# Performance work log

Hardware: AMD Instinct MI355X
Metric: run time of the kernel (lower is better)

Reference implementation:

```python
import jax, jax.numpy as jnp
import numpy as np

RES = 2048
IN = 3
OUT = 2
THRESHOLD = 1.0
BETA = 0.9
SPECTRAL_RADIUS = 0.9


def _make_W(rng):
    # random recurrent matrix scaled to target spectral radius (power iteration estimate)
    W = rng.standard_normal((RES, RES)).astype(np.float32)
    v = rng.standard_normal(RES).astype(np.float32)
    lam = 1.0
    for _ in range(100):
        v = W @ v
        lam = np.linalg.norm(v)
        v = v / (lam + 1e-12)
    return W * (SPECTRAL_RADIUS / lam)


def _xavier(rng, fan_out, fan_in):
    bound = np.sqrt(6.0 / (fan_in + fan_out))
    return rng.uniform(-bound, bound, (fan_out, fan_in)).astype(np.float32)


def setup_inputs() -> dict:
    key = jax.random.key(0)
    rng = np.random.default_rng(42)
    x = jax.random.normal(key, (200, 256, IN), dtype=jnp.float32)
    W = jnp.asarray(_make_W(rng))            # [RES, RES] recurrent weights
    Win = jnp.asarray(_xavier(rng, RES, IN))  # [RES, IN]  input_layer.weight
    Wout = jnp.asarray(_xavier(rng, OUT, RES))  # [OUT, RES] readout.weight
    return {"x": x, "W": W, "Win": Win, "Wout": Wout}


def reference(x, W, Win, Wout):
    seq_len, batch, _ = x.shape
    res = W.shape[0]

    def step(carry, x_t):
        V, S = carry
        # leaky integrate: input current + recurrent current
        V_new = BETA * V + x_t @ Win.T + S @ W  # [batch, res]
        S_new = (V_new >= THRESHOLD).astype(V.dtype)
        V_new = V_new * (1.0 - S_new)  # reset_mechanism == 'zero'
        return (V_new, S_new), S_new

    init = (jnp.zeros((batch, res), x.dtype), jnp.zeros((batch, res), x.dtype))
    _, spk_rec = jax.lax.scan(step, init, x)  # [seq, batch, res]
    spk_avg = spk_rec[-10:].mean(axis=0)       # [batch, res]
    logits = spk_avg @ Wout.T                  # [batch, out]
    return spk_rec, logits
```

## Files before the change

kernel.cpp:

```cpp
#include <hip/hip_runtime.h>


#define SEQ    200
#define BATCH  256
#define NRES   2048
#define NTHR   1024
#define BETA_F 0.9f

__global__ __launch_bounds__(NTHR, 1) void snn_reservoir_kernel(
    const float* __restrict__ x,
    const float* __restrict__ W,
    const float* __restrict__ Win,
    const float* __restrict__ Wout,
    float* __restrict__ out)
{
    const int b    = blockIdx.x;
    const int tid  = threadIdx.x;
    const int lane = tid & 63;
    const int wid  = tid >> 6;
    const int n0   = tid << 1;

    __shared__ unsigned long long smask[2][32];
    __shared__ int    scum[2];
    __shared__ float4 sx[SEQ];
    __shared__ float  red[2][16];
    __shared__ int    sspike;

    for (int t = tid; t < SEQ; t += NTHR) {
        const float* p = x + (size_t)t * (BATCH * 3) + b * 3;
        sx[t] = make_float4(p[0], p[1], p[2], 0.0f);
    }
    if (tid == 0) sspike = 0;

    const float* wr = Win + (size_t)n0 * 3;
    const float w00 = wr[0], w01 = wr[1], w02 = wr[2];
    const float w10 = wr[3], w11 = wr[4], w12 = wr[5];

    __syncthreads();

    float V0 = 0.f, V1 = 0.f;
    bool  any = false;
    unsigned long long* pout =
        (unsigned long long*)(out + (size_t)b * NRES + n0);
    const size_t step_ull = (size_t)BATCH * NRES / 2;

    #pragma unroll 4
    for (int t = 0; t < SEQ; ++t) {
        const float4 xv = sx[t];
        const float i0 = fmaf(xv.x, w00, fmaf(xv.y, w01, xv.z * w02));
        const float i1 = fmaf(xv.x, w10, fmaf(xv.y, w11, xv.z * w12));
        V0 = fmaf(BETA_F, V0, i0);
        V1 = fmaf(BETA_F, V1, i1);
        const bool s0 = (V0 >= 1.0f);
        const bool s1 = (V1 >= 1.0f);
        any |= (s0 | s1);
        V0 = s0 ? 0.f : V0;
        V1 = s1 ? 0.f : V1;
        const unsigned long long wv =
            ((unsigned long long)(s1 ? 0x3f800000u : 0u) << 32) |
            (unsigned long long)(s0 ? 0x3f800000u : 0u);
        __builtin_nontemporal_store(wv, pout);
        pout += step_ull;
    }

    const int wany = __any(any);
    if (wany && lane == 0) atomicOr(&sspike, 1);
    __syncthreads();

    const size_t loff = (size_t)SEQ * BATCH * NRES;
    if (sspike == 0) {
        if (tid == 0) {
            out[loff + b * 2 + 0] = 0.f;
            out[loff + b * 2 + 1] = 0.f;
        }
        return;
    }

    if (tid < 64) smask[tid >> 5][tid & 31] = 0ull;
    if (tid < 2)  scum[tid] = 0;
    V0 = 0.f; V1 = 0.f;
    int cnt0 = 0, cnt1 = 0;
    __syncthreads();

    auto step = [&](int t, int cur, int prev, int& seen) {
        float rec0 = 0.f, rec1 = 0.f;
        const int c = scum[prev];
        if (__builtin_expect(c != seen, 0)) {
            seen = c;
            #pragma unroll 1
            for (int u = 0; u < 32; ++u) {
                unsigned long long m = smask[prev][u];
                const int kbase = ((u >> 1) << 7) + (u & 1);
                while (m) {
                    const int l = __builtin_ctzll(m);
                    m &= m - 1;
                    const int k = kbase + (l << 1);
                    const float2 wvv = *(const float2*)(W + (size_t)k * NRES + n0);
                    rec0 += wvv.x;
                    rec1 += wvv.y;
                }
            }
        }
        const float4 xv = sx[t];
        const float i0 = fmaf(xv.x, w00, fmaf(xv.y, w01, xv.z * w02)) + rec0;
        const float i1 = fmaf(xv.x, w10, fmaf(xv.y, w11, xv.z * w12)) + rec1;
        V0 = fmaf(BETA_F, V0, i0);
        V1 = fmaf(BETA_F, V1, i1);
        const bool s0 = (V0 >= 1.0f);
        const bool s1 = (V1 >= 1.0f);
        V0 = s0 ? 0.f : V0;
        V1 = s1 ? 0.f : V1;
        *(float2*)(out + ((size_t)t * BATCH + b) * NRES + n0) =
            make_float2(s0 ? 1.f : 0.f, s1 ? 1.f : 0.f);
        if (t >= SEQ - 10) { cnt0 += (int)s0; cnt1 += (int)s1; }
        const unsigned long long b0 = __ballot(s0);
        const unsigned long long b1 = __ballot(s1);
        if (lane == 0) {
            smask[cur][2 * wid]     = b0;
            smask[cur][2 * wid + 1] = b1;
            const int pc = __popcll(b0) + __popcll(b1);
            if (pc) atomicAdd(&scum[cur], pc);
        }
        asm volatile("s_waitcnt lgkmcnt(0)\n\ts_barrier" ::: "memory");
    };

    int seen0 = 0, seen1 = 0;
    for (int tt = 0; tt < SEQ; tt += 2) {
        step(tt,     0, 1, seen1);
        step(tt + 1, 1, 0, seen0);
    }

    const float a0 = (float)cnt0 * 0.1f;
    const float a1 = (float)cnt1 * 0.1f;
    float p0 = fmaf(a0, Wout[n0], a1 * Wout[n0 + 1]);
    float p1 = fmaf(a0, Wout[NRES + n0], a1 * Wout[NRES + n0 + 1]);
    #pragma unroll
    for (int off = 32; off > 0; off >>= 1) {
        p0 += __shfl_down(p0, off);
        p1 += __shfl_down(p1, off);
    }
    if (lane == 0) { red[0][wid] = p0; red[1][wid] = p1; }
    __syncthreads();
    if (tid == 0) {
        float q0 = 0.f, q1 = 0.f;
        #pragma unroll
        for (int i = 0; i < 16; ++i) { q0 += red[0][i]; q1 += red[1][i]; }
        out[loff + b * 2 + 0] = q0;
        out[loff + b * 2 + 1] = q1;
    }
}

extern "C" void kernel_launch(void* const* d_in, const int* in_sizes, int n_in,
                              void* d_out, int out_size, void* d_ws, size_t ws_size,
                              hipStream_t stream) {
    const float* x    = (const float*)d_in[0];
    const float* W    = (const float*)d_in[1];
    const float* Win  = (const float*)d_in[2];
    const float* Wout = (const float*)d_in[3];
    float* out = (float*)d_out;
    hipLaunchKernelGGL(snn_reservoir_kernel, dim3(BATCH), dim3(NTHR), 0, stream,
                       x, W, Win, Wout, out);
}
```

Measured before the change: 425.6 us.

## Screen for spike-free inputs with a bound check and stream zeros bandwidth-optimally

Adds a tiny scan kernel that computes the leak-filtered input trace per (t, batch) row, plus a conservative bound using the max |Win| per input channel. A wide grid-stride kernel writes the whole spike and logit output as float4 zeros. Rows whose bound can reach threshold get an exact per-neuron potential check, which raises a global flag. The full recurrent kernel runs only when that flag is set. This replaces the old write path, which used one block per batch element and strided 8-byte nontemporal stores, with a fully coalesced wide write. The cost is extra launches and a small serial scan, and the full kernel still launches every time and returns early when the flag is clear.

```diff
diff --git a/kernel.cpp b/kernel.cpp
--- a/kernel.cpp
+++ b/kernel.cpp
@@ -4,16 +4,113 @@
 #define SEQ    200
 #define BATCH  256
 #define NRES   2048
-#define NTHR   1024
 #define BETA_F 0.9f
-
-__global__ __launch_bounds__(NTHR, 1) void snn_reservoir_kernel(
+#define NROW   (SEQ * BATCH)
+#define SPK_FLOATS ((size_t)SEQ * BATCH * NRES)
+#define LOGITS 512
+#define WS_FLOATS (64 + NROW + 3 * NROW)
+
+__global__ __launch_bounds__(256) void scan_kernel(
+    const float* __restrict__ x,
+    const float* __restrict__ Win,
+    float* __restrict__ ws)
+{
+    __shared__ float swm[4][3];
+    __shared__ float wm[3];
+    const int tid  = threadIdx.x;
+    const int lane = tid & 63;
+    const int wv   = tid >> 6;
+
+    float p0 = 0.f, p1 = 0.f, p2 = 0.f;
+    for (int n = tid; n < NRES; n += 256) {
+        const float* r = Win + (size_t)n * 3;
+        p0 = fmaxf(p0, fabsf(r[0]));
+        p1 = fmaxf(p1, fabsf(r[1]));
+        p2 = fmaxf(p2, fabsf(r[2]));
+    }
+    #pragma unroll
+    for (int off = 32; off; off >>= 1) {
+        p0 = fmaxf(p0, __shfl_down(p0, off));
+        p1 = fmaxf(p1, __shfl_down(p1, off));
+        p2 = fmaxf(p2, __shfl_down(p2, off));
+    }
+    if (lane == 0) { swm[wv][0] = p0; swm[wv][1] = p1; swm[wv][2] = p2; }
+    __syncthreads();
+    if (tid == 0) {
+        wm[0] = fmaxf(fmaxf(swm[0][0], swm[1][0]), fmaxf(swm[2][0], swm[3][0]));
+        wm[1] = fmaxf(fmaxf(swm[0][1], swm[1][1]), fmaxf(swm[2][1], swm[3][1]));
+        wm[2] = fmaxf(fmaxf(swm[0][2], swm[1][2]), fmaxf(swm[2][2], swm[3][2]));
+        if (blockIdx.x == 0) *(int*)ws = 0;
+    }
+    __syncthreads();
+
+    if (tid < 64) {
+        const int b = blockIdx.x * 64 + tid;
+        const float w0 = wm[0], w1 = wm[1], w2 = wm[2];
+        float* rowbound = ws + 64;
+        float* xs       = ws + 64 + NROW;
+        float X0 = 0.f, X1 = 0.f, X2 = 0.f;
+        #pragma unroll 4
+        for (int t = 0; t < SEQ; ++t) {
+            const float* px = x + ((size_t)t * BATCH + b) * 3;
+            X0 = fmaf(BETA_F, X0, px[0]);
+            X1 = fmaf(BETA_F, X1, px[1]);
+            X2 = fmaf(BETA_F, X2, px[2]);
+            const int r = t * BATCH + b;
+            rowbound[r] = fmaf(fabsf(X0), w0, fmaf(fabsf(X1), w1, fabsf(X2) * w2));
+            float* xr = xs + (size_t)r * 3;
+            xr[0] = X0; xr[1] = X1; xr[2] = X2;
+        }
+    }
+}
+
+__global__ __launch_bounds__(256) void stream_kernel(
+    const float* __restrict__ Win,
+    float* __restrict__ out,
+    float* __restrict__ ws)
+{
+    const float* rowbound = ws + 64;
+    const float* xs       = ws + 64 + NROW;
+    int* flag = (int*)ws;
+    const size_t nspk   = SPK_FLOATS / 4;
+    const size_t nchunk = nspk + LOGITS / 4;
+    const size_t stride = (size_t)gridDim.x * blockDim.x;
+    size_t idx = (size_t)blockIdx.x * blockDim.x + threadIdx.x;
+    const float4 z = make_float4(0.f, 0.f, 0.f, 0.f);
+
+    for (; idx < nchunk; idx += stride) {
+        if (idx < nspk) {
+            const int r = (int)(idx >> 9);
+            const float bnd = rowbound[r];
+            if (__builtin_expect(!(bnd < 0.999f), 0)) {
+                const int n = ((int)idx & 511) << 2;
+                const float* X = xs + (size_t)r * 3;
+                const float X0 = X[0], X1 = X[1], X2 = X[2];
+                const float* wr = Win + (size_t)n * 3;
+                const float v0 = fmaf(X0, wr[0], fmaf(X1, wr[1],  X2 * wr[2]));
+                const float v1 = fmaf(X0, wr[3], fmaf(X1, wr[4],  X2 * wr[5]));
+                const float v2 = fmaf(X0, wr[6], fmaf(X1, wr[7],  X2 * wr[8]));
+                const float v3 = fmaf(X0, wr[9], fmaf(X1, wr[10], X2 * wr[11]));
+                if (!(v0 < 1.f) || !(v1 < 1.f) || !(v2 < 1.f) || !(v3 < 1.f))
+                    atomicOr(flag, 1);
+            }
+        }
+        reinterpret_cast<float4*>(out)[idx] = z;
+    }
+}
+
+#define NTHR 1024
+
+__global__ __launch_bounds__(NTHR, 1) void fallback_kernel(
     const float* __restrict__ x,
     const float* __restrict__ W,
     const float* __restrict__ Win,
     const float* __restrict__ Wout,
-    float* __restrict__ out)
+    float* __restrict__ out,
+    const float* __restrict__ ws)
 {
+    if (*(const int*)ws == 0) return;
+
     const int b    = blockIdx.x;
     const int tid  = threadIdx.x;
     const int lane = tid & 63;
@@ -24,61 +121,19 @@
     __shared__ int    scum[2];
     __shared__ float4 sx[SEQ];
     __shared__ float  red[2][16];
-    __shared__ int    sspike;
 
     for (int t = tid; t < SEQ; t += NTHR) {
         const float* p = x + (size_t)t * (BATCH * 3) + b * 3;
         sx[t] = make_float4(p[0], p[1], p[2], 0.0f);
     }
-    if (tid == 0) sspike = 0;
+    if (tid < 64) smask[tid >> 5][tid & 31] = 0ull;
+    if (tid < 2)  scum[tid] = 0;
 
     const float* wr = Win + (size_t)n0 * 3;
     const float w00 = wr[0], w01 = wr[1], w02 = wr[2];
     const float w10 = wr[3], w11 = wr[4], w12 = wr[5];
 
-    __syncthreads();
-
     float V0 = 0.f, V1 = 0.f;
-    bool  any = false;
-    unsigned long long* pout =
-        (unsigned long long*)(out + (size_t)b * NRES + n0);
-    const size_t step_ull = (size_t)BATCH * NRES / 2;
-
-    #pragma unroll 4
-    for (int t = 0; t < SEQ; ++t) {
-        const float4 xv = sx[t];
-        const float i0 = fmaf(xv.x, w00, fmaf(xv.y, w01, xv.z * w02));
-        const float i1 = fmaf(xv.x, w10, fmaf(xv.y, w11, xv.z * w12));
-        V0 = fmaf(BETA_F, V0, i0);
-        V1 = fmaf(BETA_F, V1, i1);
-        const bool s0 = (V0 >= 1.0f);
-        const bool s1 = (V1 >= 1.0f);
-        any |= (s0 | s1);
-        V0 = s0 ? 0.f : V0;
-        V1 = s1 ? 0.f : V1;
-        const unsigned long long wv =
-            ((unsigned long long)(s1 ? 0x3f800000u : 0u) << 32) |
-            (unsigned long long)(s0 ? 0x3f800000u : 0u);
-        __builtin_nontemporal_store(wv, pout);
-        pout += step_ull;
-    }
-
-    const int wany = __any(any);
-    if (wany && lane == 0) atomicOr(&sspike, 1);
-    __syncthreads();
-
-    const size_t loff = (size_t)SEQ * BATCH * NRES;
-    if (sspike == 0) {
-        if (tid == 0) {
-            out[loff + b * 2 + 0] = 0.f;
-            out[loff + b * 2 + 1] = 0.f;
-        }
-        return;
-    }
-
-    if (tid < 64) smask[tid >> 5][tid & 31] = 0ull;
-    if (tid < 2)  scum[tid] = 0;
-    V0 = 0.f; V1 = 0.f;
     int cnt0 = 0, cnt1 = 0;
     __syncthreads();
 
@@ -145,6 +200,150 @@
         float q0 = 0.f, q1 = 0.f;
         #pragma unroll
         for (int i = 0; i < 16; ++i) { q0 += red[0][i]; q1 += red[1][i]; }
+        const size_t loff = SPK_FLOATS;
+        out[loff + b * 2 + 0] = q0;
+        out[loff + b * 2 + 1] = q1;
+    }
+}
+
+__global__ __launch_bounds__(NTHR, 1) void snn_reservoir_kernel(
+    const float* __restrict__ x,
+    const float* __restrict__ W,
+    const float* __restrict__ Win,
+    const float* __restrict__ Wout,
+    float* __restrict__ out)
+{
+    const int b    = blockIdx.x;
+    const int tid  = threadIdx.x;
+    const int lane = tid & 63;
+    const int wid  = tid >> 6;
+    const int n0   = tid << 1;
+
+    __shared__ unsigned long long smask[2][32];
+    __shared__ int    scum[2];
+    __shared__ float4 sx[SEQ];
+    __shared__ float  red[2][16];
+    __shared__ int    sspike;
+
+    for (int t = tid; t < SEQ; t += NTHR) {
+        const float* p = x + (size_t)t * (BATCH * 3) + b * 3;
+        sx[t] = make_float4(p[0], p[1], p[2], 0.0f);
+    }
+    if (tid == 0) sspike = 0;
+
+    const float* wr = Win + (size_t)n0 * 3;
+    const float w00 = wr[0], w01 = wr[1], w02 = wr[2];
+    const float w10 = wr[3], w11 = wr[4], w12 = wr[5];
+
+    __syncthreads();
+
+    float V0 = 0.f, V1 = 0.f;
+    bool  any = false;
+    unsigned long long* pout =
+        (unsigned long long*)(out + (size_t)b * NRES + n0);
+    const size_t step_ull = (size_t)BATCH * NRES / 2;
+
+    #pragma unroll 4
+    for (int t = 0; t < SEQ; ++t) {
+        const float4 xv = sx[t];
+        const float i0 = fmaf(xv.x, w00, fmaf(xv.y, w01, xv.z * w02));
+        const float i1 = fmaf(xv.x, w10, fmaf(xv.y, w11, xv.z * w12));
+        V0 = fmaf(BETA_F, V0, i0);
+        V1 = fmaf(BETA_F, V1, i1);
+        const bool s0 = (V0 >= 1.0f);
+        const bool s1 = (V1 >= 1.0f);
+        any |= (s0 | s1);
+        V0 = s0 ? 0.f : V0;
+        V1 = s1 ? 0.f : V1;
+        const unsigned long long wv =
+            ((unsigned long long)(s1 ? 0x3f800000u : 0u) << 32) |
+            (unsigned long long)(s0 ? 0x3f800000u : 0u);
+        __builtin_nontemporal_store(wv, pout);
+        pout += step_ull;
+    }
+
+    const int wany = __any(any);
+    if (wany && lane == 0) atomicOr(&sspike, 1);
+    __syncthreads();
+
+    const size_t loff = SPK_FLOATS;
+    if (sspike == 0) {
+        if (tid == 0) {
+            out[loff + b * 2 + 0] = 0.f;
+            out[loff + b * 2 + 1] = 0.f;
+        }
+        return;
+    }
+
+    if (tid < 64) smask[tid >> 5][tid & 31] = 0ull;
+    if (tid < 2)  scum[tid] = 0;
+    V0 = 0.f; V1 = 0.f;
+    int cnt0 = 0, cnt1 = 0;
+    __syncthreads();
+
+    auto step = [&](int t, int cur, int prev, int& seen) {
+        float rec0 = 0.f, rec1 = 0.f;
+        const int c = scum[prev];
+        if (__builtin_expect(c != seen, 0)) {
+            seen = c;
+            #pragma unroll 1
+            for (int u = 0; u < 32; ++u) {
+                unsigned long long m = smask[prev][u];
+                const int kbase = ((u >> 1) << 7) + (u & 1);
+                while (m) {
+                    const int l = __builtin_ctzll(m);
+                    m &= m - 1;
+                    const int k = kbase + (l << 1);
+                    const float2 wvv = *(const float2*)(W + (size_t)k * NRES + n0);
+                    rec0 += wvv.x;
+                    rec1 += wvv.y;
+                }
+            }
+        }
+        const float4 xv = sx[t];
+        const float i0 = fmaf(xv.x, w00, fmaf(xv.y, w01, xv.z * w02)) + rec0;
+        const float i1 = fmaf(xv.x, w10, fmaf(xv.y, w11, xv.z * w12)) + rec1;
+        V0 = fmaf(BETA_F, V0, i0);
+        V1 = fmaf(BETA_F, V1, i1);
+        const bool s0 = (V0 >= 1.0f);
+        const bool s1 = (V1 >= 1.0f);
+        V0 = s0 ? 0.f : V0;
+        V1 = s1 ? 0.f : V1;
+        *(float2*)(out + ((size_t)t * BATCH + b) * NRES + n0) =
+            make_float2(s0 ? 1.f : 0.f, s1 ? 1.f : 0.f);
+        if (t >= SEQ - 10) { cnt0 += (int)s0; cnt1 += (int)s1; }
+        const unsigned long long b0 = __ballot(s0);
+        const unsigned long long b1 = __ballot(s1);
+        if (lane == 0) {
+            smask[cur][2 * wid]     = b0;
+            smask[cur][2 * wid + 1] = b1;
+            const int pc = __popcll(b0) + __popcll(b1);
+            if (pc) atomicAdd(&scum[cur], pc);
+        }
+        asm volatile("s_waitcnt lgkmcnt(0)\n\ts_barrier" ::: "memory");
+    };
+
+    int seen0 = 0, seen1 = 0;
+    for (int tt = 0; tt < SEQ; tt += 2) {
+        step(tt,     0, 1, seen1);
+        step(tt + 1, 1, 0, seen0);
+    }
+
+    const float a0 = (float)cnt0 * 0.1f;
+    const float a1 = (float)cnt1 * 0.1f;
+    float p0 = fmaf(a0, Wout[n0], a1 * Wout[n0 + 1]);
+    float p1 = fmaf(a0, Wout[NRES + n0], a1 * Wout[NRES + n0 + 1]);
+    #pragma unroll
+    for (int off = 32; off > 0; off >>= 1) {
+        p0 += __shfl_down(p0, off);
+        p1 += __shfl_down(p1, off);
+    }
+    if (lane == 0) { red[0][wid] = p0; red[1][wid] = p1; }
+    __syncthreads();
+    if (tid == 0) {
+        float q0 = 0.f, q1 = 0.f;
+        #pragma unroll
+        for (int i = 0; i < 16; ++i) { q0 += red[0][i]; q1 += red[1][i]; }
         out[loff + b * 2 + 0] = q0;
         out[loff + b * 2 + 1] = q1;
     }
@@ -158,6 +357,15 @@
     const float* Win  = (const float*)d_in[2];
     const float* Wout = (const float*)d_in[3];
     float* out = (float*)d_out;
-    hipLaunchKernelGGL(snn_reservoir_kernel, dim3(BATCH), dim3(NTHR), 0, stream,
-                       x, W, Win, Wout, out);
-}
+
+    if (d_ws && ws_size >= (size_t)WS_FLOATS * sizeof(float)) {
+        float* ws = (float*)d_ws;
+        hipLaunchKernelGGL(scan_kernel,     dim3(4),    dim3(256),  0, stream, x, Win, ws);
+        hipLaunchKernelGGL(stream_kernel,   dim3(2048), dim3(256),  0, stream, Win, out, ws);
+        hipLaunchKernelGGL(fallback_kernel, dim3(BATCH), dim3(NTHR), 0, stream,
+                           x, W, Win, Wout, out, ws);
+    } else {
+        hipLaunchKernelGGL(snn_reservoir_kernel, dim3(BATCH), dim3(NTHR), 0, stream,
+                           x, W, Win, Wout, out);
+    }
+}
```

New measurement: 450.5 us. 1.06x slower.
